# Kernel tuning notes

Hardware: AMD Instinct MI355X
Metric: run time of the kernel (lower is better)

## Reference

```python
import jax, jax.numpy as jnp
import numpy as np


def setup_inputs() -> dict:
    key = jax.random.key(0)
    # [B, T_token] integer durations per phoneme token
    dur = jax.random.randint(key, (32, 4096), 0, 16, dtype=jnp.int32)
    return {"dur": dur}


def reference(dur):
    # Faithful to torch LengthRegulator.forward, but computed via segment
    # search instead of materializing the O(B, T_token, T_mel) bool mask.
    # mel2ph[b, t] = 1-based index of the token whose cumulative-duration
    # interval [cumsum_prev, cumsum) contains mel position t, else 0.
    dur = dur.astype(jnp.int32)
    dur_cumsum = jnp.cumsum(dur, axis=1)          # [B, T_token]
    total = dur_cumsum[:, -1]                     # [B] total mel frames
    T_mel = int(jnp.max(total))                   # host int (data-dependent len, as in torch)
    pos = jnp.arange(T_mel, dtype=jnp.int32)      # [T_mel]
    # searchsorted(cs, pos, 'right') == #tokens with cumsum <= pos == 0-based
    # index of containing token; matches the mask-sum semantics exactly,
    # including zero-duration tokens (they contribute empty intervals).
    tok = jax.vmap(lambda cs: jnp.searchsorted(cs, pos, side='right'))(dur_cumsum)  # [B, T_mel]
    mel2ph = jnp.where(pos[None, :] < total[:, None], tok.astype(jnp.int32) + 1, 0)
    return mel2ph
```

## Files before the change

### kernel.cpp

```cpp
#include <hip/hip_runtime.h>
#include <hip/hip_bf16.h>


#define COLS 4096
#define THREADS 256
#define CHUNK 4096
#define ITEMS 16

__global__ __launch_bounds__(THREADS) void lr_fused_kernel(
    const int* __restrict__ dur, int* __restrict__ out, int T_mel) {
    __shared__ int cs[COLS];
    __shared__ int sums[THREADS];

    const int row = blockIdx.y;
    const int t = threadIdx.x;

    const int4* d4 = reinterpret_cast<const int4*>(dur + (size_t)row * COLS) + t * 4;
    int v[ITEMS];
#pragma unroll
    for (int i = 0; i < 4; ++i) {
        int4 a = d4[i];
        v[i * 4 + 0] = a.x;
        v[i * 4 + 1] = a.y;
        v[i * 4 + 2] = a.z;
        v[i * 4 + 3] = a.w;
    }
#pragma unroll
    for (int i = 1; i < ITEMS; ++i) v[i] += v[i - 1];

    sums[t] = v[ITEMS - 1];
    __syncthreads();
#pragma unroll
    for (int off = 1; off < THREADS; off <<= 1) {
        int add = (t >= off) ? sums[t - off] : 0;
        __syncthreads();
        sums[t] += add;
        __syncthreads();
    }
    const int excl = (t == 0) ? 0 : sums[t - 1];
#pragma unroll
    for (int i = 0; i < ITEMS; ++i) cs[t * ITEMS + i] = v[i] + excl;
    __syncthreads();

    const int total = cs[COLS - 1];
    int* __restrict__ orow = out + (size_t)row * T_mel;
    const int chunk_base = blockIdx.x * CHUNK;

#pragma unroll
    for (int j = 0; j < CHUNK / THREADS; ++j) {
        const int p = chunk_base + j * THREADS + t;
        if (p >= T_mel) continue;
        int val = 0;
        if (p < total) {
            int lo = 0, hi = COLS;
#pragma unroll
            for (int s = 0; s < 12; ++s) {
                const int mid = (lo + hi) >> 1;
                const bool le = (cs[mid] <= p);
                lo = le ? mid + 1 : lo;
                hi = le ? hi : mid;
            }
            val = lo + 1;
        }
        orow[p] = val;
    }
}

extern "C" void kernel_launch(void* const* d_in, const int* in_sizes, int n_in,
                              void* d_out, int out_size, void* d_ws, size_t ws_size,
                              hipStream_t stream) {
    const int* dur = (const int*)d_in[0];
    int* out = (int*)d_out;

    const int rows = in_sizes[0] / COLS;
    const int T_mel = out_size / rows;

    dim3 grid((T_mel + CHUNK - 1) / CHUNK, rows);
    lr_fused_kernel<<<grid, THREADS, 0, stream>>>(dur, out, T_mel);
}
```

Before: 16.57 us.

## Replace per-position binary search with scatter fill into LDS chunk

Each block now scatters token indices over each token's duration range into a zero-initialised LDS copy of its output chunk, then copies the chunk out coalesced. This removes the 12-step binary search with LDS lookups per output position. The block-wide prefix scan now uses wavefront shuffles plus one small LDS exchange across the four waves, replacing the log-step shared-memory scan with its many barriers. The fill loop is variable-length per thread, which can cause wave divergence and LDS bank conflicts.

```diff
diff --git a/kernel.cpp b/kernel.cpp
--- a/kernel.cpp
+++ b/kernel.cpp
@@ -6,14 +6,18 @@
 #define THREADS 256
 #define CHUNK 4096
 #define ITEMS 16
+#define NWAVES 4
 
-__global__ __launch_bounds__(THREADS) void lr_fused_kernel(
+__global__ __launch_bounds__(THREADS) void lr_scatter_kernel(
     const int* __restrict__ dur, int* __restrict__ out, int T_mel) {
-    __shared__ int cs[COLS];
-    __shared__ int sums[THREADS];
+    __shared__ int out_lds[CHUNK];
+    __shared__ int wsum[NWAVES];
 
     const int row = blockIdx.y;
     const int t = threadIdx.x;
+    const int lane = t & 63;
+    const int wid = t >> 6;
+    const int base = blockIdx.x * CHUNK;
 
     const int4* d4 = reinterpret_cast<const int4*>(dur + (size_t)row * COLS) + t * 4;
     int v[ITEMS];
@@ -25,45 +29,53 @@
         v[i * 4 + 2] = a.z;
         v[i * 4 + 3] = a.w;
     }
+
+#pragma unroll
+    for (int j = 0; j < CHUNK / THREADS; ++j) out_lds[j * THREADS + t] = 0;
+
 #pragma unroll
     for (int i = 1; i < ITEMS; ++i) v[i] += v[i - 1];
+    const int mysum = v[ITEMS - 1];
 
-    sums[t] = v[ITEMS - 1];
-    __syncthreads();
+    int inc = mysum;
 #pragma unroll
-    for (int off = 1; off < THREADS; off <<= 1) {
-        int add = (t >= off) ? sums[t - off] : 0;
-        __syncthreads();
-        sums[t] += add;
-        __syncthreads();
+    for (int off = 1; off < 64; off <<= 1) {
+        int n = __shfl_up(inc, off, 64);
+        if (lane >= off) inc += n;
     }
-    const int excl = (t == 0) ? 0 : sums[t - 1];
-#pragma unroll
-    for (int i = 0; i < ITEMS; ++i) cs[t * ITEMS + i] = v[i] + excl;
+    if (lane == 63) wsum[wid] = inc;
     __syncthreads();
 
-    const int total = cs[COLS - 1];
+    int wbase = 0;
+#pragma unroll
+    for (int w = 0; w < NWAVES; ++w) wbase += (w < wid) ? wsum[w] : 0;
+    const int total = wsum[0] + wsum[1] + wsum[2] + wsum[3];
+    const int excl = wbase + inc - mysum;
+
+    const int chunk_end = base + CHUNK;
+    if (excl < chunk_end && excl + mysum > base) {
+        int prev = excl;
+#pragma unroll
+        for (int i = 0; i < ITEMS; ++i) {
+            const int cur = excl + v[i];
+            const int s0 = prev > base ? prev : base;
+            const int e0 = cur < chunk_end ? cur : chunk_end;
+            const int val = t * ITEMS + i + 1;
+            for (int q = s0; q < e0; ++q) out_lds[q - base] = val;
+            prev = cur;
+        }
+    }
+    __syncthreads();
+
     int* __restrict__ orow = out + (size_t)row * T_mel;
-    const int chunk_base = blockIdx.x * CHUNK;
-
+    const int limit0 = T_mel - base;
+    const int limit = limit0 < CHUNK ? limit0 : CHUNK;
 #pragma unroll
     for (int j = 0; j < CHUNK / THREADS; ++j) {
-        const int p = chunk_base + j * THREADS + t;
-        if (p >= T_mel) continue;
-        int val = 0;
-        if (p < total) {
-            int lo = 0, hi = COLS;
-#pragma unroll
-            for (int s = 0; s < 12; ++s) {
-                const int mid = (lo + hi) >> 1;
-                const bool le = (cs[mid] <= p);
-                lo = le ? mid + 1 : lo;
-                hi = le ? hi : mid;
-            }
-            val = lo + 1;
-        }
-        orow[p] = val;
+        const int idx = j * THREADS + t;
+        if (idx < limit) orow[base + idx] = out_lds[idx];
     }
+    (void)total;
 }
 
 extern "C" void kernel_launch(void* const* d_in, const int* in_sizes, int n_in,
@@ -76,5 +88,5 @@
     const int T_mel = out_size / rows;
 
     dim3 grid((T_mel + CHUNK - 1) / CHUNK, rows);
-    lr_fused_kernel<<<grid, THREADS, 0, stream>>>(dur, out, T_mel);
+    lr_scatter_kernel<<<grid, THREADS, 0, stream>>>(dur, out, T_mel);
 }
```

New measurement: 13.36 us. 1.24x faster.
